# Optimization experiments

Hardware: AMD Instinct MI355X
Metric: run time of the kernel (lower is better)

## Reference

```python
import jax, jax.numpy as jnp
import numpy as np

B, S, M, D, H, NH = 8, 1024, 2048, 512, 512, 8  # batch, seq, mem slots, memory_dim, hidden_dim, heads
THRESHOLD = 0.5
DECAY = 0.95


def setup_inputs() -> dict:
    key = jax.random.key(0)
    ks = jax.random.split(key, 16)
    def w(k, shape, s=0.02):
        return jax.random.normal(k, shape, jnp.float32) * s
    z = lambda n: jnp.zeros((n,), jnp.float32)
    return {
        'new_info': jax.random.normal(ks[0], (B, S, D), jnp.float32),
        'memory_bank': jax.random.normal(ks[1], (B, M, D), jnp.float32),
        'W_in': w(ks[2], (D, H)), 'b_in': z(H),
        'Wq': w(ks[3], (H, H)), 'bq': z(H),
        'Wk': w(ks[4], (H, H)), 'bk': z(H),
        'Wv': w(ks[5], (H, H)), 'bv': z(H),
        'Wo': w(ks[6], (H, H)), 'bo': z(H),
        'Wi1': w(ks[7], (H, H // 2)), 'bi1': z(H // 2),
        'Wi2': w(ks[8], (H // 2, 1)), 'bi2': z(1),
        'Wu1': w(ks[9], (2 * H, H)), 'bu1': z(H),
        'Wu2': w(ks[10], (H, H)), 'bu2': z(H),
    }


def _mha(q, k, v, Wq, bq, Wk, bk, Wv, bv, Wo, bo):
    # torch nn.MultiheadAttention math (batch_first, eval mode / no dropout)
    b, mq, h = q.shape
    d = h // NH
    qh = (q @ Wq + bq).reshape(b, mq, NH, d)
    kh = (k @ Wk + bk).reshape(b, -1, NH, d)
    vh = (v @ Wv + bv).reshape(b, -1, NH, d)
    scores = jnp.einsum('bqhd,bkhd->bhqk', qh, kh) / np.float32(np.sqrt(d))
    attn = jax.nn.softmax(scores, axis=-1)
    out = jnp.einsum('bhqk,bkhd->bqhd', attn, vh).reshape(b, mq, h)
    return out @ Wo + bo


def reference(new_info, memory_bank, W_in, b_in, Wq, bq, Wk, bk, Wv, bv, Wo, bo,
              Wi1, bi1, Wi2, bi2, Wu1, bu1, Wu2, bu2):
    # project new info + memory into hidden space
    info_proj = new_info @ W_in + b_in                       # [B,S,H]
    mem_proj = memory_bank @ W_in + b_in                     # [B,M,H]
    # per-token importance (sigmoid MLP)
    imp = jax.nn.sigmoid(jax.nn.relu(info_proj @ Wi1 + bi1) @ Wi2 + bi2)[..., 0]  # [B,S]
    # cross-attention: memory slots attend to new tokens -> per-slot write weights
    attn_out = _mha(mem_proj, info_proj, info_proj, Wq, bq, Wk, bk, Wv, bv, Wo, bo)  # [B,M,H]
    # scale write weights by importance (vectorized reading of the original broadcast)
    write_weights = attn_out * jnp.mean(imp, axis=1)[:, None, None]  # [B,M,H]
    # write-position selection: argmax over memory slots (importance scalar is positive,
    # so in the original all qualifying tokens of a batch pick the same slot)
    pos = jnp.argmax(jnp.mean(write_weights, axis=-1), axis=1)      # [B]
    mask = imp > THRESHOLD                                          # [B,S]
    exists = jnp.any(mask, axis=1)                                  # [B]
    # original loop overwrites the slot for each qualifying s, always reading the
    # ORIGINAL memory_bank -> final value comes from the LAST qualifying token
    s_star = S - 1 - jnp.argmax(mask[:, ::-1], axis=1)              # [B]
    bidx = jnp.arange(B)
    sel = new_info[bidx, s_star]                                    # [B,D]
    old = memory_bank[bidx, pos]                                    # [B,D]
    comb = jnp.concatenate([old, sel], axis=-1)                     # [B,2D]
    upd = jnp.tanh(jax.nn.relu(comb @ Wu1 + bu1) @ Wu2 + bu2)       # [B,H]
    ww = write_weights[bidx, pos]                                   # [B,H]
    new_mem = jnp.where(exists[:, None], old + upd * ww, old)
    updated = memory_bank.at[bidx, pos].set(new_mem)
    # forgetting: memory_age defaults to zeros -> decay_rate**0 == 1 (kept for fidelity)
    decay = jnp.power(jnp.float32(DECAY), jnp.zeros((M,), jnp.float32))
    updated = updated * decay[None, :, None]
    return updated, write_weights, imp
```

## Files before the change

### kernel.cpp

```cpp
#include <hip/hip_runtime.h>
#include <hip/hip_bf16.h>
#include <math.h>

#define BB 8
#define SS 1024
#define MM 2048
#define DD 512
#define HH 512
#define NHEAD 8
#define DHEAD 64

typedef __attribute__((ext_vector_type(8))) short short8;
typedef __attribute__((ext_vector_type(4))) float f32x4;
typedef unsigned short us;

__device__ __forceinline__ us bf_hi(float x) {
    __hip_bfloat16 h = __float2bfloat16(x);
    return *reinterpret_cast<const us*>(&h);
}
__device__ __forceinline__ float bf_f(us h) {
    return __uint_as_float(((unsigned)h) << 16);
}
__device__ __forceinline__ void split_pack4(float a, float b, float c, float d,
                                            uint2& hp, uint2& lp) {
    us h0 = bf_hi(a), h1 = bf_hi(b), h2 = bf_hi(c), h3 = bf_hi(d);
    hp.x = (unsigned)h0 | ((unsigned)h1 << 16);
    hp.y = (unsigned)h2 | ((unsigned)h3 << 16);
    us l0 = bf_hi(a - bf_f(h0)), l1 = bf_hi(b - bf_f(h1));
    us l2 = bf_hi(c - bf_f(h2)), l3 = bf_hi(d - bf_f(h3));
    lp.x = (unsigned)l0 | ((unsigned)l1 << 16);
    lp.y = (unsigned)l2 | ((unsigned)l3 << 16);
}

__device__ __forceinline__ void gload_lds16(const void* g, void* l) {
    __builtin_amdgcn_global_load_lds(
        (__attribute__((address_space(1))) void*)(g),
        (__attribute__((address_space(3))) void*)(l), 16, 0, 0);
}

__global__ __launch_bounds__(256) void prep_misc(
    const float* __restrict__ x, float* __restrict__ cpy,
    us* __restrict__ hi, us* __restrict__ lo, int n8, float* __restrict__ zbuf,
    const float* __restrict__ bk, const float* __restrict__ bv,
    float* __restrict__ bkv,
    const float* __restrict__ b_in, const float* __restrict__ Wq,
    const float* __restrict__ bq, float* __restrict__ bq_eff)
{
    const int blk = blockIdx.x, tid = threadIdx.x;
    if (blk >= 2060) {
        const int n = (blk - 2060) * 256 + tid;
        float a = bq[n];
        for (int k = 0; k < 512; ++k) a = fmaf(b_in[k], Wq[(size_t)k * 512 + n], a);
        bq_eff[n] = a;
        return;
    }
    if (blk >= 2056) {
        const int i = (blk - 2056) * 256 + tid;
        bkv[i] = (i < 512) ? bk[i] : bv[i - 512];
        return;
    }
    if (blk >= 2048) {
        const int i = (blk - 2048) * 2048 + tid * 8;
        *(float4*)(zbuf + i) = make_float4(0.f, 0.f, 0.f, 0.f);
        *(float4*)(zbuf + i + 4) = make_float4(0.f, 0.f, 0.f, 0.f);
        return;
    }
    const int stride = 2048 * 256;
    for (int i = blk * 256 + tid; i < n8; i += stride) {
        const float4 a = *(const float4*)(x + (size_t)i * 8);
        const float4 b = *(const float4*)(x + (size_t)i * 8 + 4);
        *(float4*)(cpy + (size_t)i * 8) = a;
        *(float4*)(cpy + (size_t)i * 8 + 4) = b;
        uint2 h0, l0, h1, l1;
        split_pack4(a.x, a.y, a.z, a.w, h0, l0);
        split_pack4(b.x, b.y, b.z, b.w, h1, l1);
        *(uint2*)(hi + (size_t)i * 8) = h0;
        *(uint2*)(hi + (size_t)i * 8 + 4) = h1;
        *(uint2*)(lo + (size_t)i * 8) = l0;
        *(uint2*)(lo + (size_t)i * 8 + 4) = l1;
    }
}

struct TSB {
    const float* src[6];
    us* dh[6];
    us* dl[6];
    int nc[6];
};
__global__ __launch_bounds__(256) void transpose_split_batch(TSB a)
{
    __shared__ float tile[32][33];
    const int tid = threadIdx.x;
    const int wsel = blockIdx.z;
    const int ncols = a.nc[wsel];
    const int n0 = blockIdx.x * 32, k0 = blockIdx.y * 32;
    if (n0 >= ncols) return;
    const float* W = a.src[wsel];
    {
        const int r = tid >> 3, c = (tid & 7) * 4;
        const float4 v = *(const float4*)(W + (size_t)(k0 + r) * ncols + n0 + c);
        tile[r][c + 0] = v.x; tile[r][c + 1] = v.y;
        tile[r][c + 2] = v.z; tile[r][c + 3] = v.w;
    }
    __syncthreads();
    {
        const int n = tid >> 3, k = (tid & 7) * 4;
        uint2 hp, lp;
        split_pack4(tile[k + 0][n], tile[k + 1][n], tile[k + 2][n], tile[k + 3][n], hp, lp);
        *(uint2*)(a.dh[wsel] + (size_t)(n0 + n) * 512 + k0 + k) = hp;
        *(uint2*)(a.dl[wsel] + (size_t)(n0 + n) * 512 + k0 + k) = lp;
    }
}

#define GEMM_F32A_BODY(K_)                                                          \
    __shared__ us sm[32768];                                                        \
    us* sAh = sm;            us* sAl = sm + 8192;                                   \
    us* sBh = sm + 16384;    us* sBl = sm + 24576;                                  \
    const int tid = threadIdx.x, lane = tid & 63;                                   \
    const int wid = tid >> 6, wm = wid >> 1, wn = wid & 1;                          \
    const int m0 = blockIdx.y * 128, n0 = blockIdx.x * 128;                         \
    const int fr = lane & 15, fq4 = lane >> 4;                                      \
    f32x4 acc[4][4];                                                                \
    _Pragma("unroll")                                                               \
    for (int i = 0; i < 4; ++i)                                                     \
        _Pragma("unroll")                                                           \
        for (int j = 0; j < 4; ++j)                                                 \
            _Pragma("unroll")                                                       \
            for (int r = 0; r < 4; ++r) acc[i][j][r] = 0.f;                         \
    const int ar = tid >> 4;                                                        \
    const int ak = (tid & 15) * 4;                                                  \
    int bsrow[4], bsf[4], bsoff[4];                                                 \
    _Pragma("unroll")                                                               \
    for (int it = 0; it < 4; ++it) {                                                \
        const int s = tid + 256 * it;                                               \
        bsrow[it] = s >> 3;                                                         \
        bsf[it] = s & 7;                                                            \
        bsoff[it] = bsrow[it] * 64 + ((bsf[it] ^ (bsrow[it] & 7)) << 3);            \
    }                                                                               \
    for (int k0 = 0; k0 < (K_); k0 += 64) {                                         \
        __syncthreads();                                                            \
        _Pragma("unroll")                                                           \
        for (int p = 0; p < 8; ++p) {                                               \
            const int r = p * 16 + ar;                                              \
            const float4 av = *(const float4*)(A + (size_t)(m0 + r) * (K_) + k0 + ak); \
            const int aoff = r * 128 + (((ak >> 3) ^ (r & 7)) << 4) + ((tid & 1) << 3); \
            uint2 hp, lp;                                                           \
            split_pack4(av.x, av.y, av.z, av.w, hp, lp);                            \
            *(uint2*)((char*)sAh + aoff) = hp;                                      \
            *(uint2*)((char*)sAl + aoff) = lp;                                      \
        }                                                                           \
        _Pragma("unroll")                                                           \
        for (int it = 0; it < 4; ++it) {                                            \
            const size_t bo = (size_t)(n0 + bsrow[it]) * (K_) + k0 + bsf[it] * 8;   \
            *(uint4*)(sBh + bsoff[it]) = *(const uint4*)(Bh + bo);                  \
            *(uint4*)(sBl + bsoff[it]) = *(const uint4*)(Bl + bo);                  \
        }                                                                           \
        __syncthreads();                                                            \
        _Pragma("unroll")                                                           \
        for (int ks = 0; ks < 2; ++ks) {                                            \
            short8 afh[4], afl[4], bfh[4], bfl[4];                                  \
            _Pragma("unroll")                                                       \
            for (int i = 0; i < 4; ++i) {                                           \
                const int row = wm * 64 + i * 16 + fr;                              \
                const int off = row * 128 + (((ks * 4 + fq4) ^ (row & 7)) << 4);    \
                afh[i] = *(const short8*)((const char*)sAh + off);                  \
                afl[i] = *(const short8*)((const char*)sAl + off);                  \
            }                                                                       \
            _Pragma("unroll")                                                       \
            for (int j = 0; j < 4; ++j) {                                           \
                const int row = wn * 64 + j * 16 + fr;                              \
                const int off = row * 128 + (((ks * 4 + fq4) ^ (row & 7)) << 4);    \
                bfh[j] = *(const short8*)((const char*)sBh + off);                  \
                bfl[j] = *(const short8*)((const char*)sBl + off);                  \
            }                                                                       \
            _Pragma("unroll")                                                       \
            for (int i = 0; i < 4; ++i)                                             \
                _Pragma("unroll")                                                   \
                for (int j = 0; j < 4; ++j) {                                       \
                    acc[i][j] = __builtin_amdgcn_mfma_f32_16x16x32_bf16(afh[i], bfh[j], acc[i][j], 0, 0, 0); \
                    acc[i][j] = __builtin_amdgcn_mfma_f32_16x16x32_bf16(afh[i], bfl[j], acc[i][j], 0, 0, 0); \
                    acc[i][j] = __builtin_amdgcn_mfma_f32_16x16x32_bf16(afl[i], bfh[j], acc[i][j], 0, 0, 0); \
                }                                                                   \
        }                                                                           \
    }

__global__ __launch_bounds__(256) void gemm_mfma(
    const float* __restrict__ A,
    const us* __restrict__ Bh, const us* __restrict__ Bl,
    float* __restrict__ C, int K, int N)
{
    GEMM_F32A_BODY(K)
#pragma unroll
    for (int j = 0; j < 4; ++j) {
        const int col = n0 + wn * 64 + j * 16 + fr;
#pragma unroll
        for (int i = 0; i < 4; ++i)
#pragma unroll
            for (int r = 0; r < 4; ++r) {
                const int row = m0 + wm * 64 + i * 16 + fq4 * 4 + r;
                C[(size_t)row * N + col] = acc[i][j][r];
            }
    }
}

__global__ __launch_bounds__(256) void gemm_mfma_info(
    const float* __restrict__ A,
    const us* __restrict__ Bh, const us* __restrict__ Bl,
    const float* __restrict__ bias,
    us* __restrict__ Oh, us* __restrict__ Ol)
{
    GEMM_F32A_BODY(512)
#pragma unroll
    for (int j = 0; j < 4; ++j) {
        const int col = n0 + wn * 64 + j * 16 + fr;
        const float bj = bias[col];
#pragma unroll
        for (int i = 0; i < 4; ++i)
#pragma unroll
            for (int r = 0; r < 4; ++r) {
                const int row = m0 + wm * 64 + i * 16 + fq4 * 4 + r;
                const float v = acc[i][j][r] + bj;
                const us hv = bf_hi(v);
                Oh[(size_t)row * 512 + col] = hv;
                Ol[(size_t)row * 512 + col] = bf_hi(v - bf_f(hv));
            }
    }
}

#define GEMM_PS_CORE(AhP, AlP, BhP, BlP, rsA_, K_)                                  \
    us* sAh = sm;            us* sAl = sm + 8192;                                   \
    us* sBh = sm + 16384;    us* sBl = sm + 24576;                                  \
    f32x4 acc[4][4];                                                                \
    _Pragma("unroll")                                                               \
    for (int i = 0; i < 4; ++i)                                                     \
        _Pragma("unroll")                                                           \
        for (int j = 0; j < 4; ++j)                                                 \
            _Pragma("unroll")                                                       \
            for (int r = 0; r < 4; ++r) acc[i][j][r] = 0.f;                         \
    const int fp = lane & 7, rsub = lane >> 3;                                      \
    const us* gsrc = (wid == 0) ? (AhP) : (wid == 1) ? (AlP)                        \
                   : (wid == 2) ? (BhP) : (BlP);                                    \
    const int grow0 = (wid < 2) ? m0 : n0;                                          \
    const int grs = (wid < 2) ? (rsA_) : (K_);                                      \
    us* lbase = sm + wid * 8192;                                                    \
    for (int k0 = 0; k0 < (K_); k0 += 64) {                                         \
        __syncthreads();                                                            \
        _Pragma("unroll")                                                           \
        for (int i = 0; i < 16; ++i) {                                              \
            const int row = i * 8 + rsub;                                           \
            const us* g = gsrc + (size_t)(grow0 + row) * grs + k0 +                 \
                          ((fp ^ (row & 7)) << 3);                                  \
            gload_lds16(g, lbase + i * 512);                                        \
        }                                                                           \
        __syncthreads();                                                            \
        _Pragma("unroll")                                                           \
        for (int ks = 0; ks < 2; ++ks) {                                            \
            short8 afh[4], afl[4], bfh[4], bfl[4];                                  \
            _Pragma("unroll")                                                       \
// ... 16 lines not shown
                for (int j = 0; j < 4; ++j) {                                       \
                    acc[i][j] = __builtin_amdgcn_mfma_f32_16x16x32_bf16(afh[i], bfh[j], acc[i][j], 0, 0, 0); \
                    acc[i][j] = __builtin_amdgcn_mfma_f32_16x16x32_bf16(afh[i], bfl[j], acc[i][j], 0, 0, 0); \
                    acc[i][j] = __builtin_amdgcn_mfma_f32_16x16x32_bf16(afl[i], bfh[j], acc[i][j], 0, 0, 0); \
                }                                                                   \
        }                                                                           \
    }

__global__ __launch_bounds__(256) void gemm_h1_ps(
    const us* __restrict__ Ah, const us* __restrict__ Al,
    const us* __restrict__ Bh, const us* __restrict__ Bl,
    const float* __restrict__ bias, float* __restrict__ C)
{
    __shared__ us sm[32768];
    const int tid = threadIdx.x, lane = tid & 63;
    const int wid = tid >> 6, wm = wid >> 1, wn = wid & 1;
    const int fr = lane & 15, fq4 = lane >> 4;
    const int m0 = blockIdx.y * 128, n0 = blockIdx.x * 128;
    GEMM_PS_CORE(Ah, Al, Bh, Bl, 512, 512)
#pragma unroll
    for (int j = 0; j < 4; ++j) {
        const int col = n0 + wn * 64 + j * 16 + fr;
        const float bj = bias[col];
#pragma unroll
        for (int i = 0; i < 4; ++i)
#pragma unroll
            for (int r = 0; r < 4; ++r) {
                const int row = m0 + wm * 64 + i * 16 + fq4 * 4 + r;
                C[(size_t)row * 256 + col] = fmaxf(acc[i][j][r] + bj, 0.f);
            }
    }
}

__global__ __launch_bounds__(256) void gemm_qkv_ps(
    const us* __restrict__ mbh, const us* __restrict__ mbl,
    const us* __restrict__ wtinq_h, const us* __restrict__ wtinq_l,
    const float* __restrict__ bq_eff, float* __restrict__ qout,
    const us* __restrict__ iph, const us* __restrict__ ipl,
    const us* __restrict__ wtkv_h, const us* __restrict__ wtkv_l,
    const float* __restrict__ bkv,
    us* __restrict__ Kh, us* __restrict__ Kl,
    us* __restrict__ Vth, us* __restrict__ Vtl)
{
    __shared__ us sm[32768];
    const int tid = threadIdx.x, lane = tid & 63;
    const int wid = tid >> 6, wm = wid >> 1, wn = wid & 1;
    const int fr = lane & 15, fq4 = lane >> 4;
    const int id = blockIdx.x;
    const bool isQ = (id < 512);
    int m0, n0;
    const us *Ah, *Al, *Bh, *Bl;
    if (isQ) {
        m0 = (id >> 2) * 128; n0 = (id & 3) * 128;
        Ah = mbh; Al = mbl; Bh = wtinq_h; Bl = wtinq_l;
    } else {
        const int t = id - 512;
        m0 = (t >> 3) * 128; n0 = (t & 7) * 128;
        Ah = iph; Al = ipl; Bh = wtkv_h; Bl = wtkv_l;
    }
    GEMM_PS_CORE(Ah, Al, Bh, Bl, 512, 512)

    if (isQ) {
#pragma unroll
        for (int j = 0; j < 4; ++j) {
            const int col = n0 + wn * 64 + j * 16 + fr;
            const float bj = bq_eff[col];
#pragma unroll
            for (int i = 0; i < 4; ++i)
#pragma unroll
                for (int r = 0; r < 4; ++r) {
                    const int row = m0 + wm * 64 + i * 16 + fq4 * 4 + r;
                    qout[(size_t)row * 512 + col] = acc[i][j][r] + bj;
                }
        }
    } else if (n0 < 512) {
#pragma unroll
        for (int j = 0; j < 4; ++j) {
            const int col = n0 + wn * 64 + j * 16 + fr;
            const float bj = bkv[col];
#pragma unroll
            for (int i = 0; i < 4; ++i)
#pragma unroll
                for (int r = 0; r < 4; ++r) {
                    const int row = m0 + wm * 64 + i * 16 + fq4 * 4 + r;
                    const float v = acc[i][j][r] + bj;
                    const us hv = bf_hi(v);
                    Kh[(size_t)row * 512 + col] = hv;
                    Kl[(size_t)row * 512 + col] = bf_hi(v - bf_f(hv));
                }
        }
    } else {
#pragma unroll
        for (int j = 0; j < 4; ++j) {
            const int col = n0 + wn * 64 + j * 16 + fr;
            const float bj = bkv[col];
            const int d = col - 512;
#pragma unroll
            for (int i = 0; i < 4; ++i) {
                const int row0 = m0 + wm * 64 + i * 16 + fq4 * 4;
                uint2 hp, lp;
                split_pack4(acc[i][j][0] + bj, acc[i][j][1] + bj,
                            acc[i][j][2] + bj, acc[i][j][3] + bj, hp, lp);
                const size_t vo = ((size_t)(row0 >> 10) * 512 + d) * 1024 + (row0 & 1023);
                *(uint2*)(Vth + vo) = hp;
                *(uint2*)(Vtl + vo) = lp;
            }
        }
    }
}

__global__ __launch_bounds__(256) void gemm_wo_ps(
    const us* __restrict__ Ah, const us* __restrict__ Al,
    const us* __restrict__ Bh, const us* __restrict__ Bl,
    const float* __restrict__ bias, float* __restrict__ C,
    const float* __restrict__ rowscale, float* __restrict__ rowmeanv)
{
    __shared__ us sm[32768];
    const int tid = threadIdx.x, lane = tid & 63;
// ... 7 lines not shown
    for (int i = 0; i < 4; ++i)
#pragma unroll
        for (int r = 0; r < 4; ++r) rsum[i][r] = 0.f;

#pragma unroll
    for (int j = 0; j < 4; ++j) {
        const int col = n0 + wn * 64 + j * 16 + fr;
        const float bj = bias[col];
#pragma unroll
        for (int i = 0; i < 4; ++i)
#pragma unroll
            for (int r = 0; r < 4; ++r) {
                const int row = m0 + wm * 64 + i * 16 + fq4 * 4 + r;
                const float v = (acc[i][j][r] + bj) * rowscale[row / MM];
                C[(size_t)row * 512 + col] = v;
                rsum[i][r] += v;
            }
    }

    __syncthreads();
    float* red = (float*)sm;
    if (tid < 128) red[tid] = 0.f;
    __syncthreads();
#pragma unroll
    for (int i = 0; i < 4; ++i)
#pragma unroll
        for (int r = 0; r < 4; ++r)
            atomicAdd(&red[wm * 64 + i * 16 + fq4 * 4 + r], rsum[i][r]);
    __syncthreads();
    if (tid < 128) atomicAdd(&rowmeanv[m0 + tid], red[tid] * (1.0f / 512.0f));
}

__global__ __launch_bounds__(256) void attn_mfma(
    const float* __restrict__ qh,
    const us* __restrict__ Kh, const us* __restrict__ Kl,
    const us* __restrict__ Vth, const us* __restrict__ Vtl,
    us* __restrict__ aoh, us* __restrict__ aol)
{
    __shared__ us sm[24576];
    __shared__ float sSc[64];
    us* sKh = sm;            us* sKl = sm + 4096;
    us* sVh = sm + 8192;     us* sVl = sm + 12288;
    us* sPh = sm + 16384;    us* sPl = sm + 20480;

    const int tid = threadIdx.x, lane = tid & 63, w = tid >> 6;
    const int fr = lane & 15, fq4 = lane >> 4;

    const int wg = blockIdx.x;
    const int xcd = wg & 7, ix = wg >> 3;
    const int mt = ix & 31;
    const int pair = xcd + 8 * (ix >> 5);
    const int h = pair & 7, b = pair >> 3;
    const int m0 = mt * 64;

    const float* Qg = qh + ((size_t)(b * MM + m0)) * HH + h * DHEAD;
    const us* Kgh = Kh + ((size_t)b * SS) * 512 + h * DHEAD;
    const us* Kgl = Kl + ((size_t)b * SS) * 512 + h * DHEAD;
    const us* Vgh = Vth + ((size_t)b * 512 + h * DHEAD) * 1024;
    const us* Vgl = Vtl + ((size_t)b * 512 + h * DHEAD) * 1024;
    us* Oh = aoh + ((size_t)(b * MM + m0)) * 512 + h * DHEAD;
    us* Ol = aol + ((size_t)(b * MM + m0)) * 512 + h * DHEAD;

    short8 qfh[2], qfl[2];
#pragma unroll
    for (int ks = 0; ks < 2; ++ks) {
        const float* qp = Qg + (size_t)(w * 16 + fr) * HH + ks * 32 + fq4 * 8;
        const float4 u0 = *(const float4*)qp;
        const float4 u1 = *(const float4*)(qp + 4);
        float v[8] = {u0.x, u0.y, u0.z, u0.w, u1.x, u1.y, u1.z, u1.w};
#pragma unroll
        for (int e = 0; e < 8; ++e) {
            const float x = v[e] * 0.125f;
            const us hb = bf_hi(x);
            qfh[ks][e] = (short)hb;
            qfl[ks][e] = (short)bf_hi(x - bf_f(hb));
        }
    }

    const int fp = lane & 7;
    const int rsub = lane >> 3;
    const bool isK = (w < 2);
    const us* gA = (w == 0) ? Kgh : (w == 1) ? Kgl : (w == 2) ? Vgh : Vgl;
    us* lbase = sm + w * 4096;

    f32x4 oacc[4];
#pragma unroll
    for (int j = 0; j < 4; ++j)
#pragma unroll
        for (int r = 0; r < 4; ++r) oacc[j][r] = 0.f;
    float mrun = -1e30f, lrun = 0.f;

    for (int t = 0; t < SS / 64; ++t) {
        __syncthreads();
        if (isK) {
#pragma unroll
            for (int i = 0; i < 8; ++i) {
                const int row = i * 8 + rsub;
                const us* g = gA + (size_t)(t * 64 + row) * 512 + ((fp ^ (row & 7)) << 3);
                gload_lds16(g, lbase + i * 512);
            }
        } else {
#pragma unroll
            for (int i = 0; i < 8; ++i) {
                const int row = i * 8 + rsub;
                const us* g = gA + (size_t)row * 1024 + t * 64 + ((fp ^ (row & 7)) << 3);
                gload_lds16(g, lbase + i * 512);
            }
        }
        __syncthreads();

        f32x4 stt[4];
#pragma unroll
        for (int fs = 0; fs < 4; ++fs)
#pragma unroll
            for (int r = 0; r < 4; ++r) stt[fs][r] = 0.f;
#pragma unroll
        for (int ks = 0; ks < 2; ++ks) {
            short8 kfh[4], kfl[4];
#pragma unroll
            for (int fs = 0; fs < 4; ++fs) {
                const int row = fs * 16 + fr;
                const int off = row * 128 + (((ks * 4 + fq4) ^ (row & 7)) << 4);
                kfh[fs] = *(const short8*)((const char*)sKh + off);
                kfl[fs] = *(const short8*)((const char*)sKl + off);
            }
#pragma unroll
            for (int fs = 0; fs < 4; ++fs) {
                stt[fs] = __builtin_amdgcn_mfma_f32_16x16x32_bf16(kfh[fs], qfh[ks], stt[fs], 0, 0, 0);
                stt[fs] = __builtin_amdgcn_mfma_f32_16x16x32_bf16(kfh[fs], qfl[ks], stt[fs], 0, 0, 0);
                stt[fs] = __builtin_amdgcn_mfma_f32_16x16x32_bf16(kfl[fs], qfh[ks], stt[fs], 0, 0, 0);
            }
        }

        {
            float mx = stt[0][0];
#pragma unroll
            for (int fs = 0; fs < 4; ++fs)
#pragma unroll
                for (int r = 0; r < 4; ++r) mx = fmaxf(mx, stt[fs][r]);
            mx = fmaxf(mx, __shfl_xor(mx, 16));
            mx = fmaxf(mx, __shfl_xor(mx, 32));
            const float nm = fmaxf(mrun, mx);
            const float scf = __expf(mrun - nm);
            mrun = nm;
            float ps = 0.f;
#pragma unroll
            for (int fs = 0; fs < 4; ++fs)
#pragma unroll
                for (int r = 0; r < 4; ++r) {
                    const float p = __expf(stt[fs][r] - nm);
                    stt[fs][r] = p;
                    ps += p;
                }
            ps += __shfl_xor(ps, 16);
            ps += __shfl_xor(ps, 32);
            lrun = lrun * scf + ps;
            if (fq4 == 0) sSc[w * 16 + fr] = scf;
        }

#pragma unroll
        for (int fs = 0; fs < 4; ++fs) {
            const int q = w * 16 + fr;
            const int flog = (fs << 1) | (fq4 >> 1);
            const int off = q * 128 + ((flog ^ (q & 7)) << 4) + ((fq4 & 1) << 3);
            uint2 hp, lp;
            split_pack4(stt[fs][0], stt[fs][1], stt[fs][2], stt[fs][3], hp, lp);
            *(uint2*)((char*)sPh + off) = hp;
            *(uint2*)((char*)sPl + off) = lp;
        }

#pragma unroll
        for (int r = 0; r < 4; ++r) {
            const float scv = sSc[w * 16 + fq4 * 4 + r];
#pragma unroll
            for (int fd = 0; fd < 4; ++fd) oacc[fd][r] *= scv;
        }

#pragma unroll
        for (int ks = 0; ks < 2; ++ks) {
            short8 pfh, pfl, vfh[4], vfl[4];
            {
                const int row = w * 16 + fr;
                const int off = row * 128 + (((ks * 4 + fq4) ^ (row & 7)) << 4);
                pfh = *(const short8*)((const char*)sPh + off);
                pfl = *(const short8*)((const char*)sPl + off);
            }
#pragma unroll
            for (int fd = 0; fd < 4; ++fd) {
                const int row = fd * 16 + fr;
                const int off = row * 128 + (((ks * 4 + fq4) ^ (row & 7)) << 4);
                vfh[fd] = *(const short8*)((const char*)sVh + off);
                vfl[fd] = *(const short8*)((const char*)sVl + off);
            }
#pragma unroll
            for (int fd = 0; fd < 4; ++fd) {
                oacc[fd] = __builtin_amdgcn_mfma_f32_16x16x32_bf16(pfh, vfh[fd], oacc[fd], 0, 0, 0);
                oacc[fd] = __builtin_amdgcn_mfma_f32_16x16x32_bf16(pfh, vfl[fd], oacc[fd], 0, 0, 0);
                oacc[fd] = __builtin_amdgcn_mfma_f32_16x16x32_bf16(pfl, vfh[fd], oacc[fd], 0, 0, 0);
            }
        }
    }

    if (fq4 == 0) sSc[w * 16 + fr] = lrun;
#pragma unroll
    for (int r = 0; r < 4; ++r) {
        const float inv = 1.0f / sSc[w * 16 + fq4 * 4 + r];
        const int q = w * 16 + fq4 * 4 + r;
#pragma unroll
        for (int fd = 0; fd < 4; ++fd) {
            const float v = oacc[fd][r] * inv;
            const us hv = bf_hi(v);
            Oh[(size_t)q * 512 + fd * 16 + fr] = hv;
            Ol[(size_t)q * 512 + fd * 16 + fr] = bf_hi(v - bf_f(hv));
        }
    }
}

__global__ __launch_bounds__(256) void imp_kernel(
    const float* __restrict__ h1, const float* __restrict__ Wi2,
    const float* __restrict__ bi2, float* __restrict__ imp)
{
    const int wv = threadIdx.x >> 6, lane = threadIdx.x & 63;
    const int row = blockIdx.x * 4 + wv;
    const float4 hv = *(const float4*)(h1 + (size_t)row * 256 + lane * 4);
    const float4 wvv = *(const float4*)(Wi2 + lane * 4);
    float s = hv.x * wvv.x + hv.y * wvv.y + hv.z * wvv.z + hv.w * wvv.w;
#pragma unroll
    for (int m = 1; m < 64; m <<= 1) s += __shfl_xor(s, m);
    if (lane == 0) imp[row] = 1.0f / (1.0f + expf(-(s + bi2[0])));
}

__global__ __launch_bounds__(256) void impstats_kernel(
    const float* __restrict__ imp, float* __restrict__ imp_mean,
    int* __restrict__ s_star, int* __restrict__ exists)
{
    const int b = blockIdx.x, tid = threadIdx.x;
    float sum = 0.f; int last = -1;
    for (int s = tid; s < SS; s += 256) {
        const float v = imp[b * SS + s];
        sum += v;
        if (v > 0.5f) last = s;
    }
#pragma unroll
    for (int m = 1; m < 64; m <<= 1) {
        sum += __shfl_xor(sum, m);
        last = max(last, __shfl_xor(last, m));
    }
    __shared__ float ssum[4]; __shared__ int slast[4];
    if ((tid & 63) == 0) { ssum[tid >> 6] = sum; slast[tid >> 6] = last; }
    __syncthreads();
    if (tid == 0) {
        const float t = ssum[0] + ssum[1] + ssum[2] + ssum[3];
        const int ml = max(max(slast[0], slast[1]), max(slast[2], slast[3]));
        imp_mean[b] = t / (float)SS;
        exists[b] = (ml >= 0) ? 1 : 0;
        s_star[b] = (ml >= 0) ? ml : (SS - 1);
    }
}

__global__ __launch_bounds__(256) void argmax_kernel(
    const float* __restrict__ rm, int* __restrict__ pos)
{
    const int b = blockIdx.x, tid = threadIdx.x;
    float best = -3.0e38f; int bidx = 1 << 30;
    for (int m = tid; m < MM; m += 256) {
        const float v = rm[b * MM + m];
        if (v > best || (v == best && m < bidx)) { best = v; bidx = m; }
    }
#pragma unroll
    for (int msk = 1; msk < 64; msk <<= 1) {
        const float ov = __shfl_xor(best, msk);
        const int oi = __shfl_xor(bidx, msk);
        if (ov > best || (ov == best && oi < bidx)) { best = ov; bidx = oi; }
    }
    __shared__ float sv[4]; __shared__ int si[4];
    if ((tid & 63) == 0) { sv[tid >> 6] = best; si[tid >> 6] = bidx; }
    __syncthreads();
    if (tid == 0) {
        for (int w = 1; w < 4; ++w)
            if (sv[w] > best || (sv[w] == best && si[w] < bidx)) { best = sv[w]; bidx = si[w]; }
        pos[b] = bidx;
    }
}

__global__ __launch_bounds__(256) void update_kernel(
    const float* __restrict__ mb, const float* __restrict__ ni,
    const float* __restrict__ Wu1, const float* __restrict__ bu1,
    const float* __restrict__ Wu2, const float* __restrict__ bu2,
    const float* __restrict__ wwp, const int* __restrict__ pos,
    const int* __restrict__ s_star, const int* __restrict__ exists,
    float* __restrict__ outu)
{
    const int b = blockIdx.x, tid = threadIdx.x;
    __shared__ float comb[2 * DD];
    __shared__ float hu[HH];
    const int p = pos[b], ss = s_star[b], ex = exists[b];
    const float* oldp = mb + ((size_t)(b * MM + p)) * DD;
    const float* selp = ni + ((size_t)(b * SS + ss)) * DD;
    for (int i = tid; i < DD; i += 256) { comb[i] = oldp[i]; comb[DD + i] = selp[i]; }
    __syncthreads();
#pragma unroll
    for (int t = 0; t < 2; ++t) {
        const int n = tid + t * 256;
        float a = bu1[n];
        for (int k = 0; k < 2 * DD; ++k) a = fmaf(comb[k], Wu1[(size_t)k * HH + n], a);
        hu[n] = fmaxf(a, 0.f);
    }
    __syncthreads();
#pragma unroll
    for (int t = 0; t < 2; ++t) {
        const int n = tid + t * 256;
        float a = bu2[n];
        for (int k = 0; k < HH; ++k) a = fmaf(hu[k], Wu2[(size_t)k * HH + n], a);
        const float upd = tanhf(a);
        const float wwv = wwp[((size_t)(b * MM + p)) * HH + n];
        const float ov = oldp[n];
        outu[((size_t)(b * MM + p)) * DD + n] = ex ? fmaf(upd, wwv, ov) : ov;
    }
}

extern "C" void kernel_launch(void* const* d_in, const int* in_sizes, int n_in,
                              void* d_out, int out_size, void* d_ws, size_t ws_size,
                              hipStream_t stream)
{
    const float* new_info    = (const float*)d_in[0];
    const float* memory_bank = (const float*)d_in[1];
    const float* W_in = (const float*)d_in[2];  const float* b_in = (const float*)d_in[3];
    const float* Wq   = (const float*)d_in[4];  const float* bq   = (const float*)d_in[5];
    const float* Wk   = (const float*)d_in[6];  const float* bk   = (const float*)d_in[7];
    const float* Wv   = (const float*)d_in[8];  const float* bv   = (const float*)d_in[9];
    const float* Wo   = (const float*)d_in[10]; const float* bo   = (const float*)d_in[11];
    const float* Wi1  = (const float*)d_in[12]; const float* bi1  = (const float*)d_in[13];
    const float* Wi2  = (const float*)d_in[14]; const float* bi2  = (const float*)d_in[15];
    const float* Wu1  = (const float*)d_in[16]; const float* bu1  = (const float*)d_in[17];
    const float* Wu2  = (const float*)d_in[18]; const float* bu2  = (const float*)d_in[19];

    float* out = (float*)d_out;
    float* out_updated = out;
    float* out_ww      = out + (size_t)BB * MM * HH;
    float* out_imp     = out + 2 * (size_t)BB * MM * HH;

    float* ws = (float*)d_ws;
    float* qhb       = ws;
    float* ip_sp     = qhb + 8388608;
    float* mb_sp     = ip_sp + 4194304;
    float* kvreg     = mb_sp + 8388608;
    float* winq      = kvreg + 8388608;
    float* wtf       = winq + 262144;
    float* bq_eff    = wtf + 1703936;
    float* bkv       = bq_eff + 512;
    float* rowmeanv  = bkv + 1024;
    float* imp_mean  = rowmeanv + 16384;
    int*   ipos      = (int*)(imp_mean + BB);
    int*   istar     = ipos + BB;
    int*   iexists   = istar + BB;

    float* hidden1 = qhb;

    us* iph = (us*)ip_sp;
    us* ipl = iph + 4194304;
    us* mbh = (us*)mb_sp;
    us* mbl = mbh + 8388608;
    us* Kh  = (us*)kvreg;
    us* Kl  = Kh + 4194304;
    us* Vth = Kl + 4194304;
    us* Vtl = Vth + 4194304;

    us* wtin_h  = (us*)wtf;            us* wtin_l  = wtin_h + 262144;
    us* wtq_h   = wtin_l + 262144;     us* wtq_l   = wtq_h + 262144;
    us* wtkv_h  = wtq_l + 262144;      us* wtkv_l  = wtkv_h + 524288;
    us* wto_h   = wtkv_l + 524288;     us* wto_l   = wto_h + 262144;
    us* wtinq_h = wto_l + 262144;      us* wtinq_l = wtinq_h + 262144;
    us* wti1_h  = wtinq_l + 262144;    us* wti1_l  = wti1_h + 131072;

    const dim3 blk(256);

    prep_misc<<<dim3(2062), blk, 0, stream>>>(memory_bank, out_updated,
                                              mbh, mbl, 1048576, rowmeanv,
                                              bk, bv, bkv, b_in, Wq, bq, bq_eff);

    TSB ts;
    ts.src[0] = W_in; ts.dh[0] = wtin_h;          ts.dl[0] = wtin_l;          ts.nc[0] = 512;
    ts.src[1] = Wq;   ts.dh[1] = wtq_h;           ts.dl[1] = wtq_l;           ts.nc[1] = 512;
    ts.src[2] = Wk;   ts.dh[2] = wtkv_h;          ts.dl[2] = wtkv_l;          ts.nc[2] = 512;
    ts.src[3] = Wv;   ts.dh[3] = wtkv_h + 262144; ts.dl[3] = wtkv_l + 262144; ts.nc[3] = 512;
    ts.src[4] = Wo;   ts.dh[4] = wto_h;           ts.dl[4] = wto_l;           ts.nc[4] = 512;
    ts.src[5] = Wi1;  ts.dh[5] = wti1_h;          ts.dl[5] = wti1_l;          ts.nc[5] = 256;
    transpose_split_batch<<<dim3(16, 16, 6), blk, 0, stream>>>(ts);

    gemm_mfma_info<<<dim3(4, 64), blk, 0, stream>>>(new_info, wtin_h, wtin_l,
                                                    b_in, iph, ipl);
    gemm_h1_ps<<<dim3(2, 64), blk, 0, stream>>>(iph, ipl, wti1_h, wti1_l,
                                                bi1, hidden1);
    imp_kernel<<<dim3((BB * SS) / 4), blk, 0, stream>>>(hidden1, Wi2, bi2, out_imp);
    impstats_kernel<<<dim3(BB), blk, 0, stream>>>(out_imp, imp_mean, istar, iexists);

    gemm_mfma<<<dim3(4, 4), blk, 0, stream>>>(W_in, wtq_h, wtq_l, winq, 512, 512);
    TSB ts2;
    ts2.src[0] = winq; ts2.dh[0] = wtinq_h; ts2.dl[0] = wtinq_l; ts2.nc[0] = 512;
    transpose_split_batch<<<dim3(16, 16, 1), blk, 0, stream>>>(ts2);

    gemm_qkv_ps<<<dim3(1024), blk, 0, stream>>>(mbh, mbl, wtinq_h, wtinq_l,
                                                bq_eff, qhb,
                                                iph, ipl, wtkv_h, wtkv_l, bkv,
                                                Kh, Kl, Vth, Vtl);

    attn_mfma<<<dim3(2048), blk, 0, stream>>>(qhb, Kh, Kl, Vth, Vtl, mbh, mbl);

    gemm_wo_ps<<<dim3(4, 128), blk, 0, stream>>>(mbh, mbl, wto_h, wto_l,
                                                 bo, out_ww, imp_mean, rowmeanv);

    argmax_kernel<<<dim3(BB), blk, 0, stream>>>(rowmeanv, ipos);
    update_kernel<<<dim3(BB), blk, 0, stream>>>(memory_bank, new_info,
                                                Wu1, bu1, Wu2, bu2, out_ww,
                                                ipos, istar, iexists, out_updated);
}
```

Baseline: 500.7 us.

## Fuse prep/transpose, info/winq GEMMs, imp stats, argmax+update; presplit Q; skip rescale

Merges several small launches into fewer kernels: prep plus weight transposes, the info projection GEMM plus the W_in·Wq product (written directly transposed and split), importance plus its stats, and argmax plus update. Q is emitted from the QKV GEMM as pre-split bf16 hi/lo, and the 1/8 scale is folded into K rather than applied in the attention kernel. The online softmax skips the max rescale of the output accumulator when no row max grew. This cuts launch overhead and Q traffic, at the cost of serialising imp_all over only 8 blocks and some added branch divergence.

After: 581.1 us. +16.1%, slower.

```diff
diff --git a/kernel.cpp b/kernel.cpp
--- a/kernel.cpp
+++ b/kernel.cpp
@@ -38,88 +38,81 @@
         (__attribute__((address_space(3))) void*)(l), 16, 0, 0);
 }
 
-__global__ __launch_bounds__(256) void prep_misc(
-    const float* __restrict__ x, float* __restrict__ cpy,
-    us* __restrict__ hi, us* __restrict__ lo, int n8, float* __restrict__ zbuf,
-    const float* __restrict__ bk, const float* __restrict__ bv,
-    float* __restrict__ bkv,
-    const float* __restrict__ b_in, const float* __restrict__ Wq,
-    const float* __restrict__ bq, float* __restrict__ bq_eff)
-{
-    const int blk = blockIdx.x, tid = threadIdx.x;
-    if (blk >= 2060) {
-        const int n = (blk - 2060) * 256 + tid;
-        float a = bq[n];
-        for (int k = 0; k < 512; ++k) a = fmaf(b_in[k], Wq[(size_t)k * 512 + n], a);
-        bq_eff[n] = a;
-        return;
-    }
-    if (blk >= 2056) {
-        const int i = (blk - 2056) * 256 + tid;
-        bkv[i] = (i < 512) ? bk[i] : bv[i - 512];
-        return;
-    }
-    if (blk >= 2048) {
-        const int i = (blk - 2048) * 2048 + tid * 8;
-        *(float4*)(zbuf + i) = make_float4(0.f, 0.f, 0.f, 0.f);
-        *(float4*)(zbuf + i + 4) = make_float4(0.f, 0.f, 0.f, 0.f);
-        return;
-    }
-    const int stride = 2048 * 256;
-    for (int i = blk * 256 + tid; i < n8; i += stride) {
-        const float4 a = *(const float4*)(x + (size_t)i * 8);
-        const float4 b = *(const float4*)(x + (size_t)i * 8 + 4);
-        *(float4*)(cpy + (size_t)i * 8) = a;
-        *(float4*)(cpy + (size_t)i * 8 + 4) = b;
-        uint2 h0, l0, h1, l1;
-        split_pack4(a.x, a.y, a.z, a.w, h0, l0);
-        split_pack4(b.x, b.y, b.z, b.w, h1, l1);
-        *(uint2*)(hi + (size_t)i * 8) = h0;
-        *(uint2*)(hi + (size_t)i * 8 + 4) = h1;
-        *(uint2*)(lo + (size_t)i * 8) = l0;
-        *(uint2*)(lo + (size_t)i * 8 + 4) = l1;
-    }
-}
-
 struct TSB {
     const float* src[6];
     us* dh[6];
     us* dl[6];
     int nc[6];
 };
-__global__ __launch_bounds__(256) void transpose_split_batch(TSB a)
+
+__global__ __launch_bounds__(256) void prep_all(
+    const float* __restrict__ x, float* __restrict__ cpy,
+    us* __restrict__ hi, us* __restrict__ lo, int n8, float* __restrict__ zbuf,
+    const float* __restrict__ bk, const float* __restrict__ bv,
+    float* __restrict__ bkv,
+    const float* __restrict__ b_in, const float* __restrict__ Wq,
+    const float* __restrict__ bq, float* __restrict__ bq_eff, TSB a)
 {
     __shared__ float tile[32][33];
-    const int tid = threadIdx.x;
-    const int wsel = blockIdx.z;
-    const int ncols = a.nc[wsel];
-    const int n0 = blockIdx.x * 32, k0 = blockIdx.y * 32;
-    if (n0 >= ncols) return;
-    const float* W = a.src[wsel];
-    {
-        const int r = tid >> 3, c = (tid & 7) * 4;
-        const float4 v = *(const float4*)(W + (size_t)(k0 + r) * ncols + n0 + c);
-        tile[r][c + 0] = v.x; tile[r][c + 1] = v.y;
-        tile[r][c + 2] = v.z; tile[r][c + 3] = v.w;
-    }
-    __syncthreads();
-    {
-        const int n = tid >> 3, k = (tid & 7) * 4;
-        uint2 hp, lp;
-        split_pack4(tile[k + 0][n], tile[k + 1][n], tile[k + 2][n], tile[k + 3][n], hp, lp);
-        *(uint2*)(a.dh[wsel] + (size_t)(n0 + n) * 512 + k0 + k) = hp;
-        *(uint2*)(a.dl[wsel] + (size_t)(n0 + n) * 512 + k0 + k) = lp;
+    const int blk = blockIdx.x, tid = threadIdx.x;
+    if (blk >= 2062) {
+        const int t = blk - 2062;
+        const int wsel = t >> 8;
+        const int n0 = (t & 15) * 32, k0 = ((t >> 4) & 15) * 32;
+        const int ncols = a.nc[wsel];
+        if (n0 >= ncols) return;
+        const float* W = a.src[wsel];
+        {
+            const int r = tid >> 3, c = (tid & 7) * 4;
+            const float4 v = *(const float4*)(W + (size_t)(k0 + r) * ncols + n0 + c);
+            tile[r][c + 0] = v.x; tile[r][c + 1] = v.y;
+            tile[r][c + 2] = v.z; tile[r][c + 3] = v.w;
+        }
+        __syncthreads();
+        {
+            const int n = tid >> 3, k = (tid & 7) * 4;
+            uint2 hp, lp;
+            split_pack4(tile[k + 0][n], tile[k + 1][n], tile[k + 2][n], tile[k + 3][n], hp, lp);
+            *(uint2*)(a.dh[wsel] + (size_t)(n0 + n) * 512 + k0 + k) = hp;
+            *(uint2*)(a.dl[wsel] + (size_t)(n0 + n) * 512 + k0 + k) = lp;
+        }
+        return;
+    }
+    if (blk >= 2060) {
+        const int n = (blk - 2060) * 256 + tid;
+        float v = bq[n];
+        for (int k = 0; k < 512; ++k) v = fmaf(b_in[k], Wq[(size_t)k * 512 + n], v);
+        bq_eff[n] = v;
+        return;
+    }
+    if (blk >= 2056) {
+        const int i = (blk - 2056) * 256 + tid;
+        bkv[i] = (i < 512) ? bk[i] : bv[i - 512];
+        return;
+    }
+    if (blk >= 2048) {
+        const int i = (blk - 2048) * 2048 + tid * 8;
+        *(float4*)(zbuf + i) = make_float4(0.f, 0.f, 0.f, 0.f);
+        *(float4*)(zbuf + i + 4) = make_float4(0.f, 0.f, 0.f, 0.f);
+        return;
+    }
+    const int stride = 2048 * 256;
+    for (int i = blk * 256 + tid; i < n8; i += stride) {
+        const float4 va = *(const float4*)(x + (size_t)i * 8);
+        const float4 vb = *(const float4*)(x + (size_t)i * 8 + 4);
+        *(float4*)(cpy + (size_t)i * 8) = va;
+        *(float4*)(cpy + (size_t)i * 8 + 4) = vb;
+        uint2 h0, l0, h1, l1;
+        split_pack4(va.x, va.y, va.z, va.w, h0, l0);
+        split_pack4(vb.x, vb.y, vb.z, vb.w, h1, l1);
+        *(uint2*)(hi + (size_t)i * 8) = h0;
+        *(uint2*)(hi + (size_t)i * 8 + 4) = h1;
+        *(uint2*)(lo + (size_t)i * 8) = l0;
+        *(uint2*)(lo + (size_t)i * 8 + 4) = l1;
     }
 }
 
 #define GEMM_F32A_BODY(K_)                                                          \
-    __shared__ us sm[32768];                                                        \
-    us* sAh = sm;            us* sAl = sm + 8192;                                   \
-    us* sBh = sm + 16384;    us* sBl = sm + 24576;                                  \
-    const int tid = threadIdx.x, lane = tid & 63;                                   \
-    const int wid = tid >> 6, wm = wid >> 1, wn = wid & 1;                          \
-    const int m0 = blockIdx.y * 128, n0 = blockIdx.x * 128;                         \
-    const int fr = lane & 15, fq4 = lane >> 4;                                      \
     f32x4 acc[4][4];                                                                \
     _Pragma("unroll")                                                               \
     for (int i = 0; i < 4; ++i)                                                     \
@@ -184,46 +177,67 @@
         }                                                                           \
     }
 
-__global__ __launch_bounds__(256) void gemm_mfma(
-    const float* __restrict__ A,
-    const us* __restrict__ Bh, const us* __restrict__ Bl,
-    float* __restrict__ C, int K, int N)
+__global__ __launch_bounds__(256) void gemm_info_winq(
+    const float* __restrict__ new_info,
+    const us* __restrict__ wtin_h, const us* __restrict__ wtin_l,
+    const float* __restrict__ b_in,
+    us* __restrict__ Oh, us* __restrict__ Ol,
+    const float* __restrict__ W_in,
+    const us* __restrict__ wtq_h, const us* __restrict__ wtq_l,
+    us* __restrict__ wtinq_h, us* __restrict__ wtinq_l)
 {
-    GEMM_F32A_BODY(K)
-#pragma unroll
-    for (int j = 0; j < 4; ++j) {
-        const int col = n0 + wn * 64 + j * 16 + fr;
-#pragma unroll
-        for (int i = 0; i < 4; ++i)
-#pragma unroll
-            for (int r = 0; r < 4; ++r) {
-                const int row = m0 + wm * 64 + i * 16 + fq4 * 4 + r;
-                C[(size_t)row * N + col] = acc[i][j][r];
-            }
-    }
-}
-
-__global__ __launch_bounds__(256) void gemm_mfma_info(
-    const float* __restrict__ A,
-    const us* __restrict__ Bh, const us* __restrict__ Bl,
-    const float* __restrict__ bias,
-    us* __restrict__ Oh, us* __restrict__ Ol)
-{
+    __shared__ us sm[32768];
+    us* sAh = sm;            us* sAl = sm + 8192;
+    us* sBh = sm + 16384;    us* sBl = sm + 24576;
+    const int tid = threadIdx.x, lane = tid & 63;
+    const int wid = tid >> 6, wm = wid >> 1, wn = wid & 1;
+    const int fr = lane & 15, fq4 = lane >> 4;
+    const int id = blockIdx.x;
+    const bool isInfo = (id < 256);
+    int m0, n0;
+    const float* A;
+    const us *Bh, *Bl;
+    if (isInfo) {
+        m0 = (id >> 2) * 128; n0 = (id & 3) * 128;
+        A = new_info; Bh = wtin_h; Bl = wtin_l;
+    } else {
+        const int t = id - 256;
+        m0 = (t >> 2) * 128; n0 = (t & 3) * 128;
+        A = W_in; Bh = wtq_h; Bl = wtq_l;
+    }
     GEMM_F32A_BODY(512)
-#pragma unroll
-    for (int j = 0; j < 4; ++j) {
-        const int col = n0 + wn * 64 + j * 16 + fr;
-        const float bj = bias[col];
-#pragma unroll
-        for (int i = 0; i < 4; ++i)
-#pragma unroll
-            for (int r = 0; r < 4; ++r) {
-                const int row = m0 + wm * 64 + i * 16 + fq4 * 4 + r;
-                const float v = acc[i][j][r] + bj;
-                const us hv = bf_hi(v);
-                Oh[(size_t)row * 512 + col] = hv;
-                Ol[(size_t)row * 512 + col] = bf_hi(v - bf_f(hv));
-            }
+
+    if (isInfo) {
+#pragma unroll
+        for (int j = 0; j < 4; ++j) {
+            const int col = n0 + wn * 64 + j * 16 + fr;
+            const float bj = b_in[col];
+#pragma unroll
+            for (int i = 0; i < 4; ++i)
+#pragma unroll
+                for (int r = 0; r < 4; ++r) {
+                    const int row = m0 + wm * 64 + i * 16 + fq4 * 4 + r;
+                    const float v = acc[i][j][r] + bj;
+                    const us hv = bf_hi(v);
+                    Oh[(size_t)row * 512 + col] = hv;
+                    Ol[(size_t)row * 512 + col] = bf_hi(v - bf_f(hv));
+                }
+        }
+    } else {
+#pragma unroll
+        for (int j = 0; j < 4; ++j) {
+            const int col = n0 + wn * 64 + j * 16 + fr;
+#pragma unroll
+            for (int i = 0; i < 4; ++i)
+#pragma unroll
+                for (int r = 0; r < 4; ++r) {
+                    const int row = m0 + wm * 64 + i * 16 + fq4 * 4 + r;
+                    const float v = acc[i][j][r];
+                    const us hv = bf_hi(v);
+                    wtinq_h[(size_t)col * 512 + row] = hv;
+                    wtinq_l[(size_t)col * 512 + row] = bf_hi(v - bf_f(hv));
+                }
+        }
     }
 }
 
@@ -306,10 +320,46 @@
     }
 }
 
+__global__ __launch_bounds__(256) void imp_all(
+    const float* __restrict__ h1, const float* __restrict__ Wi2,
+    const float* __restrict__ bi2, float* __restrict__ imp,
+    float* __restrict__ imp_mean, int* __restrict__ s_star,
+    int* __restrict__ exists)
+{
+    const int b = blockIdx.x, w = threadIdx.x >> 6, lane = threadIdx.x & 63;
+    const float4 wv = *(const float4*)(Wi2 + lane * 4);
+    const float b0 = bi2[0];
+    float sum = 0.f; int last = -1;
+    for (int i = 0; i < 256; ++i) {
+        const int row = b * 1024 + w + i * 4;
+        const float4 hv = *(const float4*)(h1 + (size_t)row * 256 + lane * 4);
+        float s = hv.x * wv.x + hv.y * wv.y + hv.z * wv.z + hv.w * wv.w;
+#pragma unroll
+        for (int m = 1; m < 64; m <<= 1) s += __shfl_xor(s, m);
+        const float ip = 1.0f / (1.0f + expf(-(s + b0)));
+        if (lane == 0) {
+            imp[row] = ip;
+            sum += ip;
+            if (ip > 0.5f) last = row;
+        }
+    }
+    __shared__ float ssum[4]; __shared__ int slast[4];
+    if (lane == 0) { ssum[w] = sum; slast[w] = last; }
+    __syncthreads();
+    if (threadIdx.x == 0) {
+        const float t = ssum[0] + ssum[1] + ssum[2] + ssum[3];
+        const int ml = max(max(slast[0], slast[1]), max(slast[2], slast[3]));
+        imp_mean[b] = t / (float)SS;
+        exists[b] = (ml >= 0) ? 1 : 0;
+        s_star[b] = (ml >= 0) ? (ml - b * 1024) : (SS - 1);
+    }
+}
+
 __global__ __launch_bounds__(256) void gemm_qkv_ps(
     const us* __restrict__ mbh, const us* __restrict__ mbl,
     const us* __restrict__ wtinq_h, const us* __restrict__ wtinq_l,
-    const float* __restrict__ bq_eff, float* __restrict__ qout,
+    const float* __restrict__ bq_eff,
+    us* __restrict__ qsph, us* __restrict__ qspl,
     const us* __restrict__ iph, const us* __restrict__ ipl,
     const us* __restrict__ wtkv_h, const us* __restrict__ wtkv_l,
     const float* __restrict__ bkv,
@@ -344,7 +394,10 @@
 #pragma unroll
                 for (int r = 0; r < 4; ++r) {
                     const int row = m0 + wm * 64 + i * 16 + fq4 * 4 + r;
-                    qout[(size_t)row * 512 + col] = acc[i][j][r] + bj;
+                    const float v = acc[i][j][r] + bj;
+                    const us hv = bf_hi(v);
+                    qsph[(size_t)row * 512 + col] = hv;
+                    qspl[(size_t)row * 512 + col] = bf_hi(v - bf_f(hv));
                 }
         }
     } else if (n0 < 512) {
@@ -357,7 +410,7 @@
 #pragma unroll
                 for (int r = 0; r < 4; ++r) {
                     const int row = m0 + wm * 64 + i * 16 + fq4 * 4 + r;
-                    const float v = acc[i][j][r] + bj;
+                    const float v = (acc[i][j][r] + bj) * 0.125f;
                     const us hv = bf_hi(v);
                     Kh[(size_t)row * 512 + col] = hv;
                     Kl[(size_t)row * 512 + col] = bf_hi(v - bf_f(hv));
@@ -431,7 +484,7 @@
 }
 
 __global__ __launch_bounds__(256) void attn_mfma(
-    const float* __restrict__ qh,
+    const us* __restrict__ Qh, const us* __restrict__ Ql,
     const us* __restrict__ Kh, const us* __restrict__ Kl,
     const us* __restrict__ Vth, const us* __restrict__ Vtl,
     us* __restrict__ aoh, us* __restrict__ aol)
@@ -452,7 +505,8 @@
     const int h = pair & 7, b = pair >> 3;
     const int m0 = mt * 64;
 
-    const float* Qg = qh + ((size_t)(b * MM + m0)) * HH + h * DHEAD;
+    const us* Qgh = Qh + ((size_t)(b * MM + m0)) * 512 + h * DHEAD;
+    const us* Qgl = Ql + ((size_t)(b * MM + m0)) * 512 + h * DHEAD;
     const us* Kgh = Kh + ((size_t)b * SS) * 512 + h * DHEAD;
     const us* Kgl = Kl + ((size_t)b * SS) * 512 + h * DHEAD;
     const us* Vgh = Vth + ((size_t)b * 512 + h * DHEAD) * 1024;
@@ -463,17 +517,9 @@
     short8 qfh[2], qfl[2];
 #pragma unroll
     for (int ks = 0; ks < 2; ++ks) {
-        const float* qp = Qg + (size_t)(w * 16 + fr) * HH + ks * 32 + fq4 * 8;
-        const float4 u0 = *(const float4*)qp;
-        const float4 u1 = *(const float4*)(qp + 4);
-        float v[8] = {u0.x, u0.y, u0.z, u0.w, u1.x, u1.y, u1.z, u1.w};
-#pragma unroll
-        for (int e = 0; e < 8; ++e) {
-            const float x = v[e] * 0.125f;
-            const us hb = bf_hi(x);
-            qfh[ks][e] = (short)hb;
-            qfl[ks][e] = (short)bf_hi(x - bf_f(hb));
-        }
+        const size_t qo = (size_t)(w * 16 + fr) * 512 + ks * 32 + fq4 * 8;
+        qfh[ks] = *(const short8*)(Qgh + qo);
+        qfl[ks] = *(const short8*)(Qgl + qo);
     }
 
     const int fp = lane & 7;
@@ -531,31 +577,33 @@
             }
         }
 
-        {
-            float mx = stt[0][0];
-#pragma unroll
-            for (int fs = 0; fs < 4; ++fs)
-#pragma unroll
-                for (int r = 0; r < 4; ++r) mx = fmaxf(mx, stt[fs][r]);
-            mx = fmaxf(mx, __shfl_xor(mx, 16));
-            mx = fmaxf(mx, __shfl_xor(mx, 32));
+        float mx = stt[0][0];
+#pragma unroll
+        for (int fs = 0; fs < 4; ++fs)
+#pragma unroll
+            for (int r = 0; r < 4; ++r) mx = fmaxf(mx, stt[fs][r]);
+        mx = fmaxf(mx, __shfl_xor(mx, 16));
+        mx = fmaxf(mx, __shfl_xor(mx, 32));
+        const bool grow = __any(mx > mrun);
+        float scf = 1.f;
+        if (grow) {
             const float nm = fmaxf(mrun, mx);
-            const float scf = __expf(mrun - nm);
+            scf = __expf(mrun - nm);
             mrun = nm;
-            float ps = 0.f;
-#pragma unroll
-            for (int fs = 0; fs < 4; ++fs)
-#pragma unroll
-                for (int r = 0; r < 4; ++r) {
-                    const float p = __expf(stt[fs][r] - nm);
-                    stt[fs][r] = p;
-                    ps += p;
-                }
-            ps += __shfl_xor(ps, 16);
-            ps += __shfl_xor(ps, 32);
-            lrun = lrun * scf + ps;
             if (fq4 == 0) sSc[w * 16 + fr] = scf;
         }
+        float ps = 0.f;
+#pragma unroll
+        for (int fs = 0; fs < 4; ++fs)
+#pragma unroll
+            for (int r = 0; r < 4; ++r) {
+                const float p = __expf(stt[fs][r] - mrun);
+                stt[fs][r] = p;
+                ps += p;
+            }
+        ps += __shfl_xor(ps, 16);
+        ps += __shfl_xor(ps, 32);
+        lrun = lrun * scf + ps;
 
 #pragma unroll
         for (int fs = 0; fs < 4; ++fs) {
@@ -568,11 +616,13 @@
             *(uint2*)((char*)sPl + off) = lp;
         }
 
-#pragma unroll
-        for (int r = 0; r < 4; ++r) {
-            const float scv = sSc[w * 16 + fq4 * 4 + r];
-#pragma unroll
-            for (int fd = 0; fd < 4; ++fd) oacc[fd][r] *= scv;
+        if (grow) {
+#pragma unroll
+            for (int r = 0; r < 4; ++r) {
+                const float scv = sSc[w * 16 + fq4 * 4 + r];
+#pragma unroll
+                for (int fd = 0; fd < 4; ++fd) oacc[fd][r] *= scv;
+            }
         }
 
 #pragma unroll
@@ -615,85 +665,43 @@
     }
 }
 
-__global__ __launch_bounds__(256) void imp_kernel(
-    const float* __restrict__ h1, const float* __restrict__ Wi2,
-    const float* __restrict__ bi2, float* __restrict__ imp)
-{
-    const int wv = threadIdx.x >> 6, lane = threadIdx.x & 63;
-    const int row = blockIdx.x * 4 + wv;
-    const float4 hv = *(const float4*)(h1 + (size_t)row * 256 + lane * 4);
-    const float4 wvv = *(const float4*)(Wi2 + lane * 4);
-    float s = hv.x * wvv.x + hv.y * wvv.y + hv.z * wvv.z + hv.w * wvv.w;
-#pragma unroll
-    for (int m = 1; m < 64; m <<= 1) s += __shfl_xor(s, m);
-    if (lane == 0) imp[row] = 1.0f / (1.0f + expf(-(s + bi2[0])));
-}
-
-__global__ __launch_bounds__(256) void impstats_kernel(
-    const float* __restrict__ imp, float* __restrict__ imp_mean,
-    int* __restrict__ s_star, int* __restrict__ exists)
-{
-    const int b = blockIdx.x, tid = threadIdx.x;
-    float sum = 0.f; int last = -1;
-    for (int s = tid; s < SS; s += 256) {
-        const float v = imp[b * SS + s];
-        sum += v;
-        if (v > 0.5f) last = s;
-    }
-#pragma unroll
-    for (int m = 1; m < 64; m <<= 1) {
-        sum += __shfl_xor(sum, m);
-        last = max(last, __shfl_xor(last, m));
-    }
-    __shared__ float ssum[4]; __shared__ int slast[4];
-    if ((tid & 63) == 0) { ssum[tid >> 6] = sum; slast[tid >> 6] = last; }
-    __syncthreads();
-    if (tid == 0) {
-        const float t = ssum[0] + ssum[1] + ssum[2] + ssum[3];
-        const int ml = max(max(slast[0], slast[1]), max(slast[2], slast[3]));
-        imp_mean[b] = t / (float)SS;
-        exists[b] = (ml >= 0) ? 1 : 0;
-        s_star[b] = (ml >= 0) ? ml : (SS - 1);
-    }
-}
-
-__global__ __launch_bounds__(256) void argmax_kernel(
-    const float* __restrict__ rm, int* __restrict__ pos)
-{
-    const int b = blockIdx.x, tid = threadIdx.x;
-    float best = -3.0e38f; int bidx = 1 << 30;
-    for (int m = tid; m < MM; m += 256) {
-        const float v = rm[b * MM + m];
-        if (v > best || (v == best && m < bidx)) { best = v; bidx = m; }
-    }
-#pragma unroll
-    for (int msk = 1; msk < 64; msk <<= 1) {
-        const float ov = __shfl_xor(best, msk);
-        const int oi = __shfl_xor(bidx, msk);
-        if (ov > best || (ov == best && oi < bidx)) { best = ov; bidx = oi; }
-    }
-    __shared__ float sv[4]; __shared__ int si[4];
-    if ((tid & 63) == 0) { sv[tid >> 6] = best; si[tid >> 6] = bidx; }
-    __syncthreads();
-    if (tid == 0) {
-        for (int w = 1; w < 4; ++w)
-            if (sv[w] > best || (sv[w] == best && si[w] < bidx)) { best = sv[w]; bidx = si[w]; }
-        pos[b] = bidx;
-    }
-}
-
-__global__ __launch_bounds__(256) void update_kernel(
+__global__ __launch_bounds__(256) void argmax_update(
+    const float* __restrict__ rm,
     const float* __restrict__ mb, const float* __restrict__ ni,
     const float* __restrict__ Wu1, const float* __restrict__ bu1,
     const float* __restrict__ Wu2, const float* __restrict__ bu2,
-    const float* __restrict__ wwp, const int* __restrict__ pos,
-    const int* __restrict__ s_star, const int* __restrict__ exists,
-    float* __restrict__ outu)
+    const float* __restrict__ wwp, const int* __restrict__ s_star,
+    const int* __restrict__ exists, float* __restrict__ outu)
 {
     const int b = blockIdx.x, tid = threadIdx.x;
     __shared__ float comb[2 * DD];
     __shared__ float hu[HH];
-    const int p = pos[b], ss = s_star[b], ex = exists[b];
+    __shared__ float sv[4]; __shared__ int si[4];
+    __shared__ int spos;
+
+    {
+        float best = -3.0e38f; int bidx = 1 << 30;
+        for (int m = tid; m < MM; m += 256) {
+            const float v = rm[b * MM + m];
+            if (v > best || (v == best && m < bidx)) { best = v; bidx = m; }
+        }
+#pragma unroll
+        for (int msk = 1; msk < 64; msk <<= 1) {
+            const float ov = __shfl_xor(best, msk);
+            const int oi = __shfl_xor(bidx, msk);
+            if (ov > best || (ov == best && oi < bidx)) { best = ov; bidx = oi; }
+        }
+        if ((tid & 63) == 0) { sv[tid >> 6] = best; si[tid >> 6] = bidx; }
+        __syncthreads();
+        if (tid == 0) {
+            for (int w = 1; w < 4; ++w)
+                if (sv[w] > best || (sv[w] == best && si[w] < bidx)) { best = sv[w]; bidx = si[w]; }
+            spos = bidx;
+        }
+        __syncthreads();
+    }
+
+    const int p = spos, ss = s_star[b], ex = exists[b];
     const float* oldp = mb + ((size_t)(b * MM + p)) * DD;
     const float* selp = ni + ((size_t)(b * SS + ss)) * DD;
     for (int i = tid; i < DD; i += 256) { comb[i] = oldp[i]; comb[DD + i] = selp[i]; }
@@ -740,22 +748,22 @@
     float* out_imp     = out + 2 * (size_t)BB * MM * HH;
 
     float* ws = (float*)d_ws;
-    float* qhb       = ws;
-    float* ip_sp     = qhb + 8388608;
+    float* qsp_rg    = ws;
+    float* ip_sp     = qsp_rg + 8388608;
     float* mb_sp     = ip_sp + 4194304;
     float* kvreg     = mb_sp + 8388608;
-    float* winq      = kvreg + 8388608;
-    float* wtf       = winq + 262144;
+    float* wtf       = kvreg + 8388608;
     float* bq_eff    = wtf + 1703936;
     float* bkv       = bq_eff + 512;
     float* rowmeanv  = bkv + 1024;
     float* imp_mean  = rowmeanv + 16384;
-    int*   ipos      = (int*)(imp_mean + BB);
-    int*   istar     = ipos + BB;
+    int*   istar     = (int*)(imp_mean + BB);
     int*   iexists   = istar + BB;
 
-    float* hidden1 = qhb;
-
+    float* hidden1 = qsp_rg;
+
+    us* qsph = (us*)qsp_rg;
+    us* qspl = qsph + 8388608;
     us* iph = (us*)ip_sp;
     us* ipl = iph + 4194304;
     us* mbh = (us*)mb_sp;
@@ -774,10 +782,6 @@
 
     const dim3 blk(256);
 
-    prep_misc<<<dim3(2062), blk, 0, stream>>>(memory_bank, out_updated,
-                                              mbh, mbl, 1048576, rowmeanv,
-                                              bk, bv, bkv, b_in, Wq, bq, bq_eff);
-
     TSB ts;
     ts.src[0] = W_in; ts.dh[0] = wtin_h;          ts.dl[0] = wtin_l;          ts.nc[0] = 512;
     ts.src[1] = Wq;   ts.dh[1] = wtq_h;           ts.dl[1] = wtq_l;           ts.nc[1] = 512;
@@ -785,32 +789,33 @@
     ts.src[3] = Wv;   ts.dh[3] = wtkv_h + 262144; ts.dl[3] = wtkv_l + 262144; ts.nc[3] = 512;
     ts.src[4] = Wo;   ts.dh[4] = wto_h;           ts.dl[4] = wto_l;           ts.nc[4] = 512;
     ts.src[5] = Wi1;  ts.dh[5] = wti1_h;          ts.dl[5] = wti1_l;          ts.nc[5] = 256;
-    transpose_split_batch<<<dim3(16, 16, 6), blk, 0, stream>>>(ts);
-
-    gemm_mfma_info<<<dim3(4, 64), blk, 0, stream>>>(new_info, wtin_h, wtin_l,
-                                                    b_in, iph, ipl);
+    prep_all<<<dim3(2062 + 1536), blk, 0, stream>>>(memory_bank, out_updated,
+                                                    mbh, mbl, 1048576, rowmeanv,
+                                                    bk, bv, bkv, b_in, Wq, bq,
+                                                    bq_eff, ts);
+
+    gemm_info_winq<<<dim3(272), blk, 0, stream>>>(new_info, wtin_h, wtin_l, b_in,
+                                                  iph, ipl, W_in, wtq_h, wtq_l,
+                                                  wtinq_h, wtinq_l);
+
     gemm_h1_ps<<<dim3(2, 64), blk, 0, stream>>>(iph, ipl, wti1_h, wti1_l,
                                                 bi1, hidden1);
-    imp_kernel<<<dim3((BB * SS) / 4), blk, 0, stream>>>(hidden1, Wi2, bi2, out_imp);
-    impstats_kernel<<<dim3(BB), blk, 0, stream>>>(out_imp, imp_mean, istar, iexists);
-
-    gemm_mfma<<<dim3(4, 4), blk, 0, stream>>>(W_in, wtq_h, wtq_l, winq, 512, 512);
-    TSB ts2;
-    ts2.src[0] = winq; ts2.dh[0] = wtinq_h; ts2.dl[0] = wtinq_l; ts2.nc[0] = 512;
-    transpose_split_batch<<<dim3(16, 16, 1), blk, 0, stream>>>(ts2);
+
+    imp_all<<<dim3(BB), blk, 0, stream>>>(hidden1, Wi2, bi2, out_imp,
+                                          imp_mean, istar, iexists);
 
     gemm_qkv_ps<<<dim3(1024), blk, 0, stream>>>(mbh, mbl, wtinq_h, wtinq_l,
-                                                bq_eff, qhb,
+                                                bq_eff, qsph, qspl,
                                                 iph, ipl, wtkv_h, wtkv_l, bkv,
                                                 Kh, Kl, Vth, Vtl);
 
-    attn_mfma<<<dim3(2048), blk, 0, stream>>>(qhb, Kh, Kl, Vth, Vtl, mbh, mbl);
+    attn_mfma<<<dim3(2048), blk, 0, stream>>>(qsph, qspl, Kh, Kl, Vth, Vtl,
+                                              mbh, mbl);
 
     gemm_wo_ps<<<dim3(4, 128), blk, 0, stream>>>(mbh, mbl, wto_h, wto_l,
                                                  bo, out_ww, imp_mean, rowmeanv);
 
-    argmax_kernel<<<dim3(BB), blk, 0, stream>>>(rowmeanv, ipos);
-    update_kernel<<<dim3(BB), blk, 0, stream>>>(memory_bank, new_info,
+    argmax_update<<<dim3(BB), blk, 0, stream>>>(rowmeanv, memory_bank, new_info,
                                                 Wu1, bu1, Wu2, bu2, out_ww,
-                                                ipos, istar, iexists, out_updated);
-}
+                                                istar, iexists, out_updated);
+}
```
